# Kernel tuning notes

Hardware: AMD Instinct MI355X
Metric: run time of the kernel (lower is better)

Reference implementation:

```python
import jax, jax.numpy as jnp
import numpy as np

SIM_COEFF = 25.0
COV_COEFF = 1.0
N, D = 32768, 512


def setup_inputs() -> dict:
    key = jax.random.key(0)
    k1, k2, k3 = jax.random.split(key, 3)
    z_a = jax.random.normal(k1, (N, D), dtype=jnp.float32)
    z_b = jax.random.normal(k2, (N, D), dtype=jnp.float32)
    # torch.randperm(N): values in [0, N) even though `combined` has 2N rows,
    # so both halves are drawn from z_a only (faithful to the original code).
    perm = jax.random.permutation(k3, N).astype(jnp.int32)
    return {"z_a": z_a, "z_b": z_b, "perm": perm}


def reference(z_a, z_b, perm):
    n, d = z_a.shape
    half = n // 2
    # repr (invariance) loss: MSE with mean reduction
    repr_loss = jnp.mean((z_a - z_b) ** 2)
    # combined has 2N rows but perm values < N -> selects rows of z_a
    combined = jnp.concatenate([z_a, z_b], axis=0)  # [2N, D]
    z1 = combined[perm[:half]]   # [N//2, D]
    z2 = combined[perm[half:]]   # [N - N//2, D]
    denom = jnp.float32(half - 1)  # original divides BOTH by N//2 - 1
    cov_z1 = (z1.T @ z1) / denom   # [D, D], replaces the per-sample outer-product loop
    cov_z2 = (z2.T @ z2) / denom   # [D, D]
    I = jnp.eye(d, dtype=z_a.dtype)
    cov_diff = (cov_z1 - I) @ (cov_z2 - I)
    cov_loss = jnp.sqrt(jnp.sum(cov_diff ** 2))  # Frobenius norm
    return SIM_COEFF * repr_loss + COV_COEFF * cov_loss
```

## Files before the change

### kernel.cpp

```cpp
#include <hip/hip_runtime.h>
#include <math.h>

typedef unsigned short u16;
typedef __attribute__((ext_vector_type(8))) short s16x8;
typedef __attribute__((ext_vector_type(4))) float f32x4;

#define NROWS 32768
#define DDIM 512
#define HALF 16384
#define KB 64
#define CSLICE 4
#define NSLICE 32
#define NSLOG2 5

__device__ __forceinline__ u16 f2bf(float f) {
  unsigned int u = __float_as_uint(f);
  unsigned int rounding = 0x7FFFu + ((u >> 16) & 1u);
  u += rounding;
  return (u16)(u >> 16);
}

__device__ __forceinline__ float bf2f(u16 h) {
  return __uint_as_float(((unsigned)h) << 16);
}

__device__ __forceinline__ void block_atomic_sum(float v, float* dst) {
  #pragma unroll
  for (int o = 32; o > 0; o >>= 1) v += __shfl_down(v, o);
  __shared__ float red[4];
  int w = threadIdx.x >> 6;
  if ((threadIdx.x & 63) == 0) red[w] = v;
  __syncthreads();
  if (threadIdx.x == 0) atomicAdd(dst, red[0] + red[1] + red[2] + red[3]);
}

__global__ void inv_kernel(const int* __restrict__ perm, int* __restrict__ inv) {
  int i = blockIdx.x * 256 + threadIdx.x;
  inv[perm[i]] = i;
}

__device__ __forceinline__ float chunk_proc(float4 a0, float4 a1, float4 b0, float4 b1,
                                            int r, int c8, u16* z1, u16* z2) {
  uint4 o;
  o.x = (unsigned)f2bf(a0.x) | ((unsigned)f2bf(a0.y) << 16);
  o.y = (unsigned)f2bf(a0.z) | ((unsigned)f2bf(a0.w) << 16);
  o.z = (unsigned)f2bf(a1.x) | ((unsigned)f2bf(a1.y) << 16);
  o.w = (unsigned)f2bf(a1.z) | ((unsigned)f2bf(a1.w) << 16);
  u16* dst = (r < HALF) ? (z1 + (size_t)r * DDIM + c8) : (z2 + (size_t)(r - HALF) * DDIM + c8);
  *reinterpret_cast<uint4*>(dst) = o;
  float dx = a0.x - b0.x, dy = a0.y - b0.y, dz = a0.z - b0.z, dw = a0.w - b0.w;
  float ex = a1.x - b1.x, ey = a1.y - b1.y, ez = a1.z - b1.z, ew = a1.w - b1.w;
  return dx*dx + dy*dy + dz*dz + dw*dw + ex*ex + ey*ey + ez*ez + ew*ew;
}

__global__ __launch_bounds__(256) void scatter_repr_kernel(
    const float* __restrict__ za, const float* __restrict__ zb, const int* __restrict__ inv,
    u16* __restrict__ z1, u16* __restrict__ z2, float* __restrict__ sums) {
  int t = threadIdx.x;
  int ch0 = (0 * 2048 + blockIdx.x) * 256 + t;
  int ch1 = (1 * 2048 + blockIdx.x) * 256 + t;
  int ch2 = (2 * 2048 + blockIdx.x) * 256 + t;
  int ch3 = (3 * 2048 + blockIdx.x) * 256 + t;
  int row0 = ch0 >> 6, row1 = ch1 >> 6, row2 = ch2 >> 6, row3 = ch3 >> 6;
  int c80 = (ch0 & 63) << 3, c81 = (ch1 & 63) << 3, c82 = (ch2 & 63) << 3, c83 = (ch3 & 63) << 3;
  const float4* pa0 = reinterpret_cast<const float4*>(za + (size_t)row0 * DDIM + c80);
  const float4* pa1 = reinterpret_cast<const float4*>(za + (size_t)row1 * DDIM + c81);
  const float4* pa2 = reinterpret_cast<const float4*>(za + (size_t)row2 * DDIM + c82);
  const float4* pa3 = reinterpret_cast<const float4*>(za + (size_t)row3 * DDIM + c83);
  const float4* pb0 = reinterpret_cast<const float4*>(zb + (size_t)row0 * DDIM + c80);
  const float4* pb1 = reinterpret_cast<const float4*>(zb + (size_t)row1 * DDIM + c81);
  const float4* pb2 = reinterpret_cast<const float4*>(zb + (size_t)row2 * DDIM + c82);
  const float4* pb3 = reinterpret_cast<const float4*>(zb + (size_t)row3 * DDIM + c83);
  float4 a00 = pa0[0], a01 = pa0[1];
  float4 a10 = pa1[0], a11 = pa1[1];
  float4 a20 = pa2[0], a21 = pa2[1];
  float4 a30 = pa3[0], a31 = pa3[1];
  float4 b00 = pb0[0], b01 = pb0[1];
  float4 b10 = pb1[0], b11 = pb1[1];
  float4 b20 = pb2[0], b21 = pb2[1];
  float4 b30 = pb3[0], b31 = pb3[1];
  int r0 = inv[row0], r1 = inv[row1], r2 = inv[row2], r3 = inv[row3];
  asm volatile("" :: "v"(a00.x), "v"(a01.x), "v"(a10.x), "v"(a11.x),
                     "v"(a20.x), "v"(a21.x), "v"(a30.x), "v"(a31.x),
                     "v"(b00.x), "v"(b01.x), "v"(b10.x), "v"(b11.x),
                     "v"(b20.x), "v"(b21.x), "v"(b30.x), "v"(b31.x),
                     "v"(r0), "v"(r1), "v"(r2), "v"(r3));
  float acc = 0.0f;
  acc += chunk_proc(a00, a01, b00, b01, r0, c80, z1, z2);
  acc += chunk_proc(a10, a11, b10, b11, r1, c81, z1, z2);
  acc += chunk_proc(a20, a21, b20, b21, r2, c82, z1, z2);
  acc += chunk_proc(a30, a31, b30, b31, r3, c83, z1, z2);
  block_atomic_sum(acc, &sums[0]);
}

__device__ __forceinline__ int swz(int col) { return (((col >> 3) + col) & 7) << 3; }

__device__ __forceinline__ void store8(u16* lds, int c0, int kp, uint4 v0, uint4 v1) {
  const ushort* h0 = reinterpret_cast<const ushort*>(&v0);
  const ushort* h1 = reinterpret_cast<const ushort*>(&v1);
  #pragma unroll
  for (int j = 0; j < 8; ++j) {
    int col = c0 + j;
    unsigned w = (unsigned)h0[j] | ((unsigned)h1[j] << 16);
    *reinterpret_cast<unsigned*>(lds + col * KB + ((kp ^ swz(col)))) = w;
  }
}

__global__ __launch_bounds__(256) void gram_kernel(const u16* __restrict__ z1,
                                                   const u16* __restrict__ z2,
                                                   u16* __restrict__ parts) {
  int b = blockIdx.x;
  int mat = b & 1;
  int rest = b >> 1;
  int slice = rest & (NSLICE - 1);
  int tile = rest >> NSLOG2;
  int bi, bj;
  if (tile < 4)      { bi = 0; bj = tile; }
  else if (tile < 7) { bi = 1; bj = tile - 3; }
  else if (tile < 9) { bi = 2; bj = tile - 5; }
  else               { bi = 3; bj = 3; }
  int ti = bi * 128, tj = bj * 128;
  const u16* Z = mat ? z2 : z1;
  bool dual = (ti != tj);
  u16* P = parts + ((size_t)(mat * NSLICE + slice)) * (DDIM * DDIM);

  __shared__ u16 ldsA[128 * KB];
  __shared__ u16 ldsB[128 * KB];
  const u16* ldsBp = dual ? ldsB : ldsA;

  int t = threadIdx.x;
  int lane = t & 63;
  int wave = t >> 6;
  int wrow = (wave >> 1) * 64;
  int wcol = (wave & 1) * 64;
  int g = lane >> 4;
  int c = lane & 15;
  int h = lane >> 4;
  int c0 = (lane & 15) << 3;
  int kp0 = 8 * wave + 2 * h;

  f32x4 acc[4][4];
  #pragma unroll
  for (int m = 0; m < 4; ++m)
    #pragma unroll
    for (int n = 0; n < 4; ++n)
      #pragma unroll
      for (int r = 0; r < 4; ++r) acc[m][n][r] = 0.0f;

  uint4 xa0, xa1, xa2, xa3, xb0, xb1, xb2, xb3;
  uint4 ya0, ya1, ya2, ya3, yb0, yb1, yb2, yb3;

#define GLOAD(p, kkv) { \
    const u16* s0 = Z + (size_t)((kkv) + kp0) * DDIM; \
    const u16* s1 = Z + (size_t)((kkv) + kp0 + 32) * DDIM; \
    p##a0 = *reinterpret_cast<const uint4*>(s0 + ti + c0); \
    p##a1 = *reinterpret_cast<const uint4*>(s0 + DDIM + ti + c0); \
    p##a2 = *reinterpret_cast<const uint4*>(s1 + ti + c0); \
    p##a3 = *reinterpret_cast<const uint4*>(s1 + DDIM + ti + c0); \
    if (dual) { \
      p##b0 = *reinterpret_cast<const uint4*>(s0 + tj + c0); \
      p##b1 = *reinterpret_cast<const uint4*>(s0 + DDIM + tj + c0); \
      p##b2 = *reinterpret_cast<const uint4*>(s1 + tj + c0); \
      p##b3 = *reinterpret_cast<const uint4*>(s1 + DDIM + tj + c0); \
    } }

#define GSTORE(p) { \
    store8(ldsA, c0, kp0, p##a0, p##a1); \
    store8(ldsA, c0, kp0 + 32, p##a2, p##a3); \
    if (dual) { \
      store8(ldsB, c0, kp0, p##b0, p##b1); \
      store8(ldsB, c0, kp0 + 32, p##b2, p##b3); \
    } }

#define COMPUTE() { \
    _Pragma("unroll") \
    for (int ks = 0; ks < KB; ks += 32) { \
      s16x8 afr[4], bfr[4]; \
      _Pragma("unroll") \
      for (int m = 0; m < 4; ++m) { \
        int colA = wrow + m * 16 + c; \
        afr[m] = *reinterpret_cast<const s16x8*>(ldsA + colA * KB + ((ks + 8 * g) ^ swz(colA))); \
        int colB = wcol + m * 16 + c; \
        bfr[m] = *reinterpret_cast<const s16x8*>(ldsBp + colB * KB + ((ks + 8 * g) ^ swz(colB))); \
      } \
      _Pragma("unroll") \
      for (int m = 0; m < 4; ++m) \
        _Pragma("unroll") \
        for (int n = 0; n < 4; ++n) \
          acc[m][n] = __builtin_amdgcn_mfma_f32_16x16x32_bf16(afr[m], bfr[n], acc[m][n], 0, 0, 0); \
    } }

  const int kspan = HALF >> NSLOG2;
  const int k0 = slice * kspan;
  GLOAD(x, k0);
  for (int kk = k0; kk < k0 + kspan; kk += 2 * KB) {
    __syncthreads();
    GSTORE(x);
    __syncthreads();
    GLOAD(y, kk + KB);
    COMPUTE();
    __syncthreads();
    GSTORE(y);
    __syncthreads();
    if (kk + 2 * KB < k0 + kspan) GLOAD(x, kk + 2 * KB);
    COMPUTE();
  }
#undef GLOAD
#undef GSTORE
#undef COMPUTE

  #pragma unroll
  for (int m = 0; m < 4; ++m)
    #pragma unroll
    for (int n = 0; n < 4; ++n)
      #pragma unroll
      for (int r = 0; r < 4; ++r) {
        int orow = ti + wrow + m * 16 + 4 * g + r;
        int ocol = tj + wcol + n * 16 + c;
        P[orow * DDIM + ocol] = f2bf(acc[m][n][r]);
      }
}

__global__ void reduce_parts_kernel(const u16* __restrict__ parts, float* __restrict__ cov) {
  int idx = blockIdx.x * 256 + threadIdx.x;
  int mat = (idx >= 40960) ? 1 : 0;
  int tl = idx - mat * 40960;
  int region = tl >> 12;
  int o = tl & 4095;
  int bi, bj;
  if (region < 4)      { bi = 0; bj = region; }
  else if (region < 7) { bi = 1; bj = region - 3; }
  else if (region < 9) { bi = 2; bj = region - 5; }
  else                 { bi = 3; bj = 3; }
  int r = bi * 128 + (o >> 5);
  int cc = bj * 128 + ((o & 31) << 2);
  const u16* base = parts + (size_t)mat * NSLICE * (DDIM * DDIM);
  float sx = 0.f, sy = 0.f, sz = 0.f, sw = 0.f;
  #pragma unroll 4
  for (int j = 0; j < NSLICE; ++j) {
    ushort4 v = *reinterpret_cast<const ushort4*>(base + (size_t)j * (DDIM * DDIM) + r * DDIM + cc);
    sx += bf2f(v.x); sy += bf2f(v.y); sz += bf2f(v.z); sw += bf2f(v.w);
  }
  const float inv = 1.0f / 16383.0f;
  sx *= inv; sy *= inv; sz *= inv; sw *= inv;
  float* cv = cov + (size_t)mat * (DDIM * DDIM);
  float4 ov; ov.x = sx; ov.y = sy; ov.z = sz; ov.w = sw;
  *reinterpret_cast<float4*>(cv + r * DDIM + cc) = ov;
  if (bi != bj) {
    cv[(cc + 0) * DDIM + r] = sx;
    cv[(cc + 1) * DDIM + r] = sy;
    cv[(cc + 2) * DDIM + r] = sz;
    cv[(cc + 3) * DDIM + r] = sw;
  }
}

__global__ __launch_bounds__(256) void covdiff_part_kernel(const float* __restrict__ cov,
                                                           float* __restrict__ pcov) {
  int bid = blockIdx.x;
  int bx = bid & 15, by = (bid >> 4) & 15, sl = bid >> 8;
  int r0 = by * 32, c0 = bx * 32, ks = sl * 128;
  const float* c1 = cov;
  const float* c2 = cov + DDIM * DDIM;
  __shared__ float ldsA[32 * 132];
  __shared__ float ldsB[128 * 33];
  int t = threadIdx.x;
  #pragma unroll
  for (int j = 0; j < 4; ++j) {
    int f4 = t + 256 * j;
    int row = f4 >> 5;
    int k4 = (f4 & 31) << 2;
    float4 v = *reinterpret_cast<const float4*>(c1 + (size_t)(r0 + row) * DDIM + ks + k4);
    int gr = r0 + row;
    if (gr == ks + k4 + 0) v.x -= 1.f;
    if (gr == ks + k4 + 1) v.y -= 1.f;
    if (gr == ks + k4 + 2) v.z -= 1.f;
    if (gr == ks + k4 + 3) v.w -= 1.f;
    *reinterpret_cast<float4*>(&ldsA[row * 132 + k4]) = v;
  }
  {
    int c = t & 31;
    int kb = t >> 5;
    #pragma unroll
    for (int j = 0; j < 16; ++j) {
      int k = kb + 8 * j;
      float v = c2[(size_t)(ks + k) * DDIM + c0 + c];
      if (ks + k == c0 + c) v -= 1.f;
      ldsB[k * 33 + c] = v;
    }
  }
  __syncthreads();
  int col = t & 31;
  int ty = t >> 5;
  float e0 = 0.f, e1 = 0.f, e2 = 0.f, e3 = 0.f;
  #pragma unroll 4
  for (int k = 0; k < 128; ++k) {
    float bv = ldsB[k * 33 + col];
    e0 = fmaf(ldsA[(ty * 4 + 0) * 132 + k], bv, e0);
    e1 = fmaf(ldsA[(ty * 4 + 1) * 132 + k], bv, e1);
    e2 = fmaf(ldsA[(ty * 4 + 2) * 132 + k], bv, e2);
    e3 = fmaf(ldsA[(ty * 4 + 3) * 132 + k], bv, e3);
  }
  float* P = pcov + (size_t)sl * (DDIM * DDIM);
  P[(r0 + ty * 4 + 0) * DDIM + c0 + col] = e0;
  P[(r0 + ty * 4 + 1) * DDIM + c0 + col] = e1;
  P[(r0 + ty * 4 + 2) * DDIM + c0 + col] = e2;
  P[(r0 + ty * 4 + 3) * DDIM + c0 + col] = e3;
}

__global__ void covred_kernel(const float* __restrict__ pcov, float* __restrict__ sums) {
  int idx = blockIdx.x * 256 + threadIdx.x;
  float sx = 0.f, sy = 0.f, sz = 0.f, sw = 0.f;
  #pragma unroll
  for (int j = 0; j < CSLICE; ++j) {
    float4 v = reinterpret_cast<const float4*>(pcov)[idx + j * 65536];
    sx += v.x; sy += v.y; sz += v.z; sw += v.w;
  }
  float q = sx * sx + sy * sy + sz * sz + sw * sw;
  block_atomic_sum(q, &sums[1]);
}

__global__ void finalize_kernel(const float* __restrict__ sums, float* __restrict__ out) {
  if (threadIdx.x == 0 && blockIdx.x == 0)
    out[0] = 25.0f * (sums[0] / 16777216.0f) + sqrtf(sums[1]);
}

extern "C" void kernel_launch(void* const* d_in, const int* in_sizes, int n_in,
                              void* d_out, int out_size, void* d_ws, size_t ws_size,
                              hipStream_t stream) {
  const float* za = (const float*)d_in[0];
  const float* zb = (const float*)d_in[1];
  const int* perm = (const int*)d_in[2];
  float* out = (float*)d_out;
  char* ws = (char*)d_ws;

  float* sums = (float*)ws;
  u16* parts = (u16*)(ws + 256);
  size_t off = 256 + (size_t)2 * NSLICE * DDIM * DDIM * 2;
  float* cov = (float*)(ws + off);
  off += (size_t)2 * DDIM * DDIM * 4;
  u16* z1 = (u16*)(ws + off);
  u16* z2 = z1 + (size_t)HALF * DDIM;
  float* pcov = (float*)z1;
  off += (size_t)2 * HALF * DDIM * 2;
  int* inv = (int*)(ws + off);

  (void)hipMemsetAsync(ws, 0, 256, stream);
  inv_kernel<<<NROWS / 256, 256, 0, stream>>>(perm, inv);
  scatter_repr_kernel<<<2048, 256, 0, stream>>>(za, zb, inv, z1, z2, sums);
  gram_kernel<<<2 * 10 * NSLICE, 256, 0, stream>>>(z1, z2, parts);
  reduce_parts_kernel<<<320, 256, 0, stream>>>(parts, cov);
  covdiff_part_kernel<<<16 * 16 * CSLICE, 256, 0, stream>>>(cov, pcov);
  covred_kernel<<<256, 256, 0, stream>>>(pcov, sums);
  finalize_kernel<<<1, 64, 0, stream>>>(sums, out);
}
```

Measured before the change: 94.41 us.

## Replace row scatter with masked Gram: cov2 = full Gram minus masked Gram

Drops the inverse-permutation scatter and converts z_a to bf16 in place, sequentially. A bitmask marks the rows selected by perm[:half]. The Gram kernel then accumulates the full Gram and the masked Gram together in one pass, and cov2 is recovered as their difference. This removes the scattered writes and the separate per-matrix Gram launches, at the cost of doubling the MFMA work per k-step, running K over all rows, and a subtraction of bf16-rounded partials that may lose precision. The slice count is chosen to fit the workspace size.

```diff
diff --git a/kernel.cpp b/kernel.cpp
--- a/kernel.cpp
+++ b/kernel.cpp
@@ -2,6 +2,7 @@
 #include <math.h>
 
 typedef unsigned short u16;
+typedef unsigned char u8;
 typedef __attribute__((ext_vector_type(8))) short s16x8;
 typedef __attribute__((ext_vector_type(4))) float f32x4;
 
@@ -10,8 +11,6 @@
 #define HALF 16384
 #define KB 64
 #define CSLICE 4
-#define NSLICE 32
-#define NSLOG2 5
 
 __device__ __forceinline__ u16 f2bf(float f) {
   unsigned int u = __float_as_uint(f);
@@ -34,63 +33,35 @@
   if (threadIdx.x == 0) atomicAdd(dst, red[0] + red[1] + red[2] + red[3]);
 }
 
-__global__ void inv_kernel(const int* __restrict__ perm, int* __restrict__ inv) {
+__global__ __launch_bounds__(256) void repr_convert_kernel(
+    const float* __restrict__ za, const float* __restrict__ zb,
+    u16* __restrict__ zc, float* __restrict__ sums) {
+  int t = blockIdx.x * 256 + threadIdx.x;
+  float acc = 0.0f;
+  #pragma unroll
+  for (int i = 0; i < 4; ++i) {
+    size_t e0 = ((size_t)(i * 524288 + t)) * 8;
+    const float4* pa = reinterpret_cast<const float4*>(za + e0);
+    const float4* pb = reinterpret_cast<const float4*>(zb + e0);
+    float4 a0 = pa[0], a1 = pa[1];
+    float4 b0 = pb[0], b1 = pb[1];
+    uint4 o;
+    o.x = (unsigned)f2bf(a0.x) | ((unsigned)f2bf(a0.y) << 16);
+    o.y = (unsigned)f2bf(a0.z) | ((unsigned)f2bf(a0.w) << 16);
+    o.z = (unsigned)f2bf(a1.x) | ((unsigned)f2bf(a1.y) << 16);
+    o.w = (unsigned)f2bf(a1.z) | ((unsigned)f2bf(a1.w) << 16);
+    *reinterpret_cast<uint4*>(zc + e0) = o;
+    float dx = a0.x - b0.x, dy = a0.y - b0.y, dz = a0.z - b0.z, dw = a0.w - b0.w;
+    float ex = a1.x - b1.x, ey = a1.y - b1.y, ez = a1.z - b1.z, ew = a1.w - b1.w;
+    acc += dx*dx + dy*dy + dz*dz + dw*dw + ex*ex + ey*ey + ez*ez + ew*ew;
+  }
+  block_atomic_sum(acc, &sums[0]);
+}
+
+__global__ void mask_kernel(const int* __restrict__ perm, unsigned* __restrict__ mbits) {
   int i = blockIdx.x * 256 + threadIdx.x;
-  inv[perm[i]] = i;
-}
-
-__device__ __forceinline__ float chunk_proc(float4 a0, float4 a1, float4 b0, float4 b1,
-                                            int r, int c8, u16* z1, u16* z2) {
-  uint4 o;
-  o.x = (unsigned)f2bf(a0.x) | ((unsigned)f2bf(a0.y) << 16);
-  o.y = (unsigned)f2bf(a0.z) | ((unsigned)f2bf(a0.w) << 16);
-  o.z = (unsigned)f2bf(a1.x) | ((unsigned)f2bf(a1.y) << 16);
-  o.w = (unsigned)f2bf(a1.z) | ((unsigned)f2bf(a1.w) << 16);
-  u16* dst = (r < HALF) ? (z1 + (size_t)r * DDIM + c8) : (z2 + (size_t)(r - HALF) * DDIM + c8);
-  *reinterpret_cast<uint4*>(dst) = o;
-  float dx = a0.x - b0.x, dy = a0.y - b0.y, dz = a0.z - b0.z, dw = a0.w - b0.w;
-  float ex = a1.x - b1.x, ey = a1.y - b1.y, ez = a1.z - b1.z, ew = a1.w - b1.w;
-  return dx*dx + dy*dy + dz*dz + dw*dw + ex*ex + ey*ey + ez*ez + ew*ew;
-}
-
-__global__ __launch_bounds__(256) void scatter_repr_kernel(
-    const float* __restrict__ za, const float* __restrict__ zb, const int* __restrict__ inv,
-    u16* __restrict__ z1, u16* __restrict__ z2, float* __restrict__ sums) {
-  int t = threadIdx.x;
-  int ch0 = (0 * 2048 + blockIdx.x) * 256 + t;
-  int ch1 = (1 * 2048 + blockIdx.x) * 256 + t;
-  int ch2 = (2 * 2048 + blockIdx.x) * 256 + t;
-  int ch3 = (3 * 2048 + blockIdx.x) * 256 + t;
-  int row0 = ch0 >> 6, row1 = ch1 >> 6, row2 = ch2 >> 6, row3 = ch3 >> 6;
-  int c80 = (ch0 & 63) << 3, c81 = (ch1 & 63) << 3, c82 = (ch2 & 63) << 3, c83 = (ch3 & 63) << 3;
-  const float4* pa0 = reinterpret_cast<const float4*>(za + (size_t)row0 * DDIM + c80);
-  const float4* pa1 = reinterpret_cast<const float4*>(za + (size_t)row1 * DDIM + c81);
-  const float4* pa2 = reinterpret_cast<const float4*>(za + (size_t)row2 * DDIM + c82);
-  const float4* pa3 = reinterpret_cast<const float4*>(za + (size_t)row3 * DDIM + c83);
-  const float4* pb0 = reinterpret_cast<const float4*>(zb + (size_t)row0 * DDIM + c80);
-  const float4* pb1 = reinterpret_cast<const float4*>(zb + (size_t)row1 * DDIM + c81);
-  const float4* pb2 = reinterpret_cast<const float4*>(zb + (size_t)row2 * DDIM + c82);
-  const float4* pb3 = reinterpret_cast<const float4*>(zb + (size_t)row3 * DDIM + c83);
-  float4 a00 = pa0[0], a01 = pa0[1];
-  float4 a10 = pa1[0], a11 = pa1[1];
-  float4 a20 = pa2[0], a21 = pa2[1];
-  float4 a30 = pa3[0], a31 = pa3[1];
-  float4 b00 = pb0[0], b01 = pb0[1];
-  float4 b10 = pb1[0], b11 = pb1[1];
-  float4 b20 = pb2[0], b21 = pb2[1];
-  float4 b30 = pb3[0], b31 = pb3[1];
-  int r0 = inv[row0], r1 = inv[row1], r2 = inv[row2], r3 = inv[row3];
-  asm volatile("" :: "v"(a00.x), "v"(a01.x), "v"(a10.x), "v"(a11.x),
-                     "v"(a20.x), "v"(a21.x), "v"(a30.x), "v"(a31.x),
-                     "v"(b00.x), "v"(b01.x), "v"(b10.x), "v"(b11.x),
-                     "v"(b20.x), "v"(b21.x), "v"(b30.x), "v"(b31.x),
-                     "v"(r0), "v"(r1), "v"(r2), "v"(r3));
-  float acc = 0.0f;
-  acc += chunk_proc(a00, a01, b00, b01, r0, c80, z1, z2);
-  acc += chunk_proc(a10, a11, b10, b11, r1, c81, z1, z2);
-  acc += chunk_proc(a20, a21, b20, b21, r2, c82, z1, z2);
-  acc += chunk_proc(a30, a31, b30, b31, r3, c83, z1, z2);
-  block_atomic_sum(acc, &sums[0]);
+  int p = perm[i];
+  atomicOr(&mbits[p >> 5], 1u << (p & 31));
 }
 
 __device__ __forceinline__ int swz(int col) { return (((col >> 3) + col) & 7) << 3; }
@@ -106,26 +77,26 @@
   }
 }
 
-__global__ __launch_bounds__(256) void gram_kernel(const u16* __restrict__ z1,
-                                                   const u16* __restrict__ z2,
-                                                   u16* __restrict__ parts) {
+__global__ __launch_bounds__(256) void gram_kernel(const u16* __restrict__ zc,
+                                                   const u8* __restrict__ mbytes,
+                                                   u16* __restrict__ parts,
+                                                   int ns, int nslog2) {
   int b = blockIdx.x;
-  int mat = b & 1;
-  int rest = b >> 1;
-  int slice = rest & (NSLICE - 1);
-  int tile = rest >> NSLOG2;
+  int slice = b & (ns - 1);
+  int tile = b >> nslog2;
   int bi, bj;
   if (tile < 4)      { bi = 0; bj = tile; }
   else if (tile < 7) { bi = 1; bj = tile - 3; }
   else if (tile < 9) { bi = 2; bj = tile - 5; }
   else               { bi = 3; bj = 3; }
   int ti = bi * 128, tj = bj * 128;
-  const u16* Z = mat ? z2 : z1;
   bool dual = (ti != tj);
-  u16* P = parts + ((size_t)(mat * NSLICE + slice)) * (DDIM * DDIM);
+  u16* P1 = parts + (size_t)slice * (DDIM * DDIM);
+  u16* Pa = parts + ((size_t)ns + slice) * (DDIM * DDIM);
 
   __shared__ u16 ldsA[128 * KB];
   __shared__ u16 ldsB[128 * KB];
+  __shared__ unsigned mlds[32];
   const u16* ldsBp = dual ? ldsB : ldsA;
 
   int t = threadIdx.x;
@@ -139,20 +110,21 @@
   int c0 = (lane & 15) << 3;
   int kp0 = 8 * wave + 2 * h;
 
-  f32x4 acc[4][4];
+  f32x4 acc1[4][4], acca[4][4];
   #pragma unroll
   for (int m = 0; m < 4; ++m)
     #pragma unroll
     for (int n = 0; n < 4; ++n)
       #pragma unroll
-      for (int r = 0; r < 4; ++r) acc[m][n][r] = 0.0f;
+      for (int r = 0; r < 4; ++r) { acc1[m][n][r] = 0.0f; acca[m][n][r] = 0.0f; }
 
   uint4 xa0, xa1, xa2, xa3, xb0, xb1, xb2, xb3;
   uint4 ya0, ya1, ya2, ya3, yb0, yb1, yb2, yb3;
+  unsigned mx = 0, my = 0;
 
 #define GLOAD(p, kkv) { \
-    const u16* s0 = Z + (size_t)((kkv) + kp0) * DDIM; \
-    const u16* s1 = Z + (size_t)((kkv) + kp0 + 32) * DDIM; \
+    const u16* s0 = zc + (size_t)((kkv) + kp0) * DDIM; \
+    const u16* s1 = zc + (size_t)((kkv) + kp0 + 32) * DDIM; \
     p##a0 = *reinterpret_cast<const uint4*>(s0 + ti + c0); \
     p##a1 = *reinterpret_cast<const uint4*>(s0 + DDIM + ti + c0); \
     p##a2 = *reinterpret_cast<const uint4*>(s1 + ti + c0); \
@@ -162,7 +134,8 @@
       p##b1 = *reinterpret_cast<const uint4*>(s0 + DDIM + tj + c0); \
       p##b2 = *reinterpret_cast<const uint4*>(s1 + tj + c0); \
       p##b3 = *reinterpret_cast<const uint4*>(s1 + DDIM + tj + c0); \
-    } }
+    } \
+    if (t < 8) m##p = mbytes[((kkv) >> 3) + t]; }
 
 #define GSTORE(p) { \
     store8(ldsA, c0, kp0, p##a0, p##a1); \
@@ -170,6 +143,13 @@
     if (dual) { \
       store8(ldsB, c0, kp0, p##b0, p##b1); \
       store8(ldsB, c0, kp0 + 32, p##b2, p##b3); \
+    } \
+    if (t < 8) { \
+      unsigned bb = m##p; \
+      _Pragma("unroll") \
+      for (int e = 0; e < 4; ++e) \
+        mlds[t * 4 + e] = (((bb >> (2 * e)) & 1) ? 0x0000FFFFu : 0u) | \
+                          (((bb >> (2 * e + 1)) & 1) ? 0xFFFF0000u : 0u); \
     } }
 
 #define COMPUTE() { \
@@ -183,14 +163,21 @@
         int colB = wcol + m * 16 + c; \
         bfr[m] = *reinterpret_cast<const s16x8*>(ldsBp + colB * KB + ((ks + 8 * g) ^ swz(colB))); \
       } \
+      uint4 mw = *reinterpret_cast<const uint4*>(&mlds[((ks >> 5) * 4 + g) * 4]); \
       _Pragma("unroll") \
-      for (int m = 0; m < 4; ++m) \
+      for (int m = 0; m < 4; ++m) { \
+        uint4 ua = *reinterpret_cast<uint4*>(&afr[m]); \
+        ua.x &= mw.x; ua.y &= mw.y; ua.z &= mw.z; ua.w &= mw.w; \
+        s16x8 am = *reinterpret_cast<s16x8*>(&ua); \
         _Pragma("unroll") \
-        for (int n = 0; n < 4; ++n) \
-          acc[m][n] = __builtin_amdgcn_mfma_f32_16x16x32_bf16(afr[m], bfr[n], acc[m][n], 0, 0, 0); \
+        for (int n = 0; n < 4; ++n) { \
+          acca[m][n] = __builtin_amdgcn_mfma_f32_16x16x32_bf16(afr[m], bfr[n], acca[m][n], 0, 0, 0); \
+          acc1[m][n] = __builtin_amdgcn_mfma_f32_16x16x32_bf16(am, bfr[n], acc1[m][n], 0, 0, 0); \
+        } \
+      } \
     } }
 
-  const int kspan = HALF >> NSLOG2;
+  const int kspan = NROWS >> nslog2;
   const int k0 = slice * kspan;
   GLOAD(x, k0);
   for (int kk = k0; kk < k0 + kspan; kk += 2 * KB) {
@@ -217,16 +204,16 @@
       for (int r = 0; r < 4; ++r) {
         int orow = ti + wrow + m * 16 + 4 * g + r;
         int ocol = tj + wcol + n * 16 + c;
-        P[orow * DDIM + ocol] = f2bf(acc[m][n][r]);
+        P1[orow * DDIM + ocol] = f2bf(acc1[m][n][r]);
+        Pa[orow * DDIM + ocol] = f2bf(acca[m][n][r]);
       }
 }
 
-__global__ void reduce_parts_kernel(const u16* __restrict__ parts, float* __restrict__ cov) {
+__global__ void reduce_parts_kernel(const u16* __restrict__ parts, float* __restrict__ cov,
+                                    int ns) {
   int idx = blockIdx.x * 256 + threadIdx.x;
-  int mat = (idx >= 40960) ? 1 : 0;
-  int tl = idx - mat * 40960;
-  int region = tl >> 12;
-  int o = tl & 4095;
+  int region = idx >> 12;
+  int o = idx & 4095;
   int bi, bj;
   if (region < 4)      { bi = 0; bj = region; }
   else if (region < 7) { bi = 1; bj = region - 3; }
@@ -234,23 +221,35 @@
   else                 { bi = 3; bj = 3; }
   int r = bi * 128 + (o >> 5);
   int cc = bj * 128 + ((o & 31) << 2);
-  const u16* base = parts + (size_t)mat * NSLICE * (DDIM * DDIM);
-  float sx = 0.f, sy = 0.f, sz = 0.f, sw = 0.f;
+  size_t pos = (size_t)r * DDIM + cc;
+  float s1x = 0.f, s1y = 0.f, s1z = 0.f, s1w = 0.f;
+  float sax = 0.f, say = 0.f, saz = 0.f, saw = 0.f;
   #pragma unroll 4
-  for (int j = 0; j < NSLICE; ++j) {
-    ushort4 v = *reinterpret_cast<const ushort4*>(base + (size_t)j * (DDIM * DDIM) + r * DDIM + cc);
-    sx += bf2f(v.x); sy += bf2f(v.y); sz += bf2f(v.z); sw += bf2f(v.w);
+  for (int j = 0; j < ns; ++j) {
+    ushort4 v1 = *reinterpret_cast<const ushort4*>(parts + (size_t)j * (DDIM * DDIM) + pos);
+    ushort4 va = *reinterpret_cast<const ushort4*>(parts + (size_t)(ns + j) * (DDIM * DDIM) + pos);
+    s1x += bf2f(v1.x); s1y += bf2f(v1.y); s1z += bf2f(v1.z); s1w += bf2f(v1.w);
+    sax += bf2f(va.x); say += bf2f(va.y); saz += bf2f(va.z); saw += bf2f(va.w);
   }
   const float inv = 1.0f / 16383.0f;
-  sx *= inv; sy *= inv; sz *= inv; sw *= inv;
-  float* cv = cov + (size_t)mat * (DDIM * DDIM);
-  float4 ov; ov.x = sx; ov.y = sy; ov.z = sz; ov.w = sw;
-  *reinterpret_cast<float4*>(cv + r * DDIM + cc) = ov;
+  float c1x = s1x * inv, c1y = s1y * inv, c1z = s1z * inv, c1w = s1w * inv;
+  float c2x = (sax - s1x) * inv, c2y = (say - s1y) * inv;
+  float c2z = (saz - s1z) * inv, c2w = (saw - s1w) * inv;
+  float* cv1 = cov;
+  float* cv2 = cov + DDIM * DDIM;
+  float4 o1; o1.x = c1x; o1.y = c1y; o1.z = c1z; o1.w = c1w;
+  float4 o2; o2.x = c2x; o2.y = c2y; o2.z = c2z; o2.w = c2w;
+  *reinterpret_cast<float4*>(cv1 + pos) = o1;
+  *reinterpret_cast<float4*>(cv2 + pos) = o2;
   if (bi != bj) {
-    cv[(cc + 0) * DDIM + r] = sx;
-    cv[(cc + 1) * DDIM + r] = sy;
-    cv[(cc + 2) * DDIM + r] = sz;
-    cv[(cc + 3) * DDIM + r] = sw;
+    cv1[(cc + 0) * DDIM + r] = c1x;
+    cv1[(cc + 1) * DDIM + r] = c1y;
+    cv1[(cc + 2) * DDIM + r] = c1z;
+    cv1[(cc + 3) * DDIM + r] = c1w;
+    cv2[(cc + 0) * DDIM + r] = c2x;
+    cv2[(cc + 1) * DDIM + r] = c2y;
+    cv2[(cc + 2) * DDIM + r] = c2z;
+    cv2[(cc + 3) * DDIM + r] = c2w;
   }
 }
 
@@ -333,22 +332,29 @@
   float* out = (float*)d_out;
   char* ws = (char*)d_ws;
 
+  const size_t covOff = 8192;
+  const size_t zcOff = covOff + (size_t)2 * DDIM * DDIM * 4;
+  const size_t partsOff = zcOff + (size_t)NROWS * DDIM * 2;
+  int nslog2 = 6;
+  while (nslog2 > 3) {
+    size_t need = partsOff + (((size_t)2 * DDIM * DDIM * 2) << nslog2);
+    if (need <= ws_size) break;
+    nslog2--;
+  }
+  int ns = 1 << nslog2;
+
   float* sums = (float*)ws;
-  u16* parts = (u16*)(ws + 256);
-  size_t off = 256 + (size_t)2 * NSLICE * DDIM * DDIM * 2;
-  float* cov = (float*)(ws + off);
-  off += (size_t)2 * DDIM * DDIM * 4;
-  u16* z1 = (u16*)(ws + off);
-  u16* z2 = z1 + (size_t)HALF * DDIM;
-  float* pcov = (float*)z1;
-  off += (size_t)2 * HALF * DDIM * 2;
-  int* inv = (int*)(ws + off);
-
-  (void)hipMemsetAsync(ws, 0, 256, stream);
-  inv_kernel<<<NROWS / 256, 256, 0, stream>>>(perm, inv);
-  scatter_repr_kernel<<<2048, 256, 0, stream>>>(za, zb, inv, z1, z2, sums);
-  gram_kernel<<<2 * 10 * NSLICE, 256, 0, stream>>>(z1, z2, parts);
-  reduce_parts_kernel<<<320, 256, 0, stream>>>(parts, cov);
+  unsigned* mbits = (unsigned*)(ws + 256);
+  float* cov = (float*)(ws + covOff);
+  u16* zc = (u16*)(ws + zcOff);
+  u16* parts = (u16*)(ws + partsOff);
+  float* pcov = (float*)zc;
+
+  (void)hipMemsetAsync(ws, 0, 4352, stream);
+  repr_convert_kernel<<<2048, 256, 0, stream>>>(za, zb, zc, sums);
+  mask_kernel<<<HALF / 256, 256, 0, stream>>>(perm, mbits);
+  gram_kernel<<<10 * ns, 256, 0, stream>>>(zc, (const u8*)mbits, parts, ns, nslog2);
+  reduce_parts_kernel<<<160, 256, 0, stream>>>(parts, cov, ns);
   covdiff_part_kernel<<<16 * 16 * CSLICE, 256, 0, stream>>>(cov, pcov);
   covred_kernel<<<256, 256, 0, stream>>>(pcov, sums);
   finalize_kernel<<<1, 64, 0, stream>>>(sums, out);
```

Measured after the change: 113.9 us. 1.21x slower.
